# Kernel tuning notes

Hardware: AMD Instinct MI355X
Metric: run time of the kernel (lower is better)

Reference implementation:

```python
import jax, jax.numpy as jnp
import numpy as np
from functools import partial

B, S, V, H, NH, NKV, M, L = 2, 2048, 51200, 1536, 24, 4, 8960, 8
DH = H // NH  # 64
EPS = 1e-6


def setup_inputs() -> dict:
    key = jax.random.key(0)
    ks = jax.random.split(key, 16)
    sc = 0.02
    w = lambda k, shape: jax.random.normal(k, shape, jnp.float32) * sc
    inp = {
        "input_ids": jax.random.randint(ks[0], (B, S), 0, V),
        "attention_mask": jnp.ones((B, S), jnp.float32),
        "embed": w(ks[1], (V, H)),
        "Wq": w(ks[2], (L, H, H)),          "bq": jnp.zeros((L, H), jnp.float32),
        "Wk": w(ks[3], (L, H, NKV * DH)),   "bk": jnp.zeros((L, NKV * DH), jnp.float32),
        "Wv": w(ks[4], (L, H, NKV * DH)),   "bv": jnp.zeros((L, NKV * DH), jnp.float32),
        "Wo": w(ks[5], (L, H, H)),
        "ln1": jnp.ones((L, H), jnp.float32),
        "ln2": jnp.ones((L, H), jnp.float32),
        "Wg": w(ks[6], (L, H, M)),
        "Wu": w(ks[7], (L, H, M)),
        "Wd": w(ks[8], (L, M, H)),
        "norm_w": jnp.ones((H,), jnp.float32),
        "W1": w(ks[9], (H, H)), "b1": jnp.zeros((H,), jnp.float32),
        "W2": w(ks[10], (H, 1)), "b2": jnp.zeros((1,), jnp.float32),
    }
    inv_freq = 1.0 / (10000.0 ** (jnp.arange(0, DH, 2, dtype=jnp.float32) / DH))
    freqs = jnp.outer(jnp.arange(S, dtype=jnp.float32), inv_freq)  # [S, DH/2]
    emb = jnp.concatenate([freqs, freqs], axis=-1)                 # [S, DH]
    inp["cos"] = jnp.cos(emb)
    inp["sin"] = jnp.sin(emb)
    return inp


def _rms(x, w):
    var = jnp.mean(x.astype(jnp.float32) ** 2, axis=-1, keepdims=True)
    return w * (x * jax.lax.rsqrt(var + EPS)).astype(x.dtype)


def _rotate_half(x):
    x1, x2 = jnp.split(x, 2, axis=-1)
    return jnp.concatenate([-x2, x1], axis=-1)


def _forward(input_ids, attention_mask, embed, Wq, bq, Wk, bk, Wv, bv, Wo,
             ln1, ln2, Wg, Wu, Wd, norm_w, W1, b1, W2, b2, cos, sin):
    scale = 1.0 / np.sqrt(DH)
    b, s = input_ids.shape
    c = cos[None, :s, None, :]  # [1,S,1,DH]
    sn = sin[None, :s, None, :]
    rope = lambda t: t * c + _rotate_half(t) * sn
    mask0 = attention_mask[:, None, None, :] == 0  # [B,1,1,S]

    def block(x, p):
        wq, bq_, wk, bk_, wv, bv_, wo, ln1w, ln2w, wg, wu, wd = p
        h = _rms(x, ln1w)
        q = (h @ wq + bq_).reshape(b, s, NH, DH)
        k = (h @ wk + bk_).reshape(b, s, NKV, DH)
        v = (h @ wv + bv_).reshape(b, s, NKV, DH)
        q, k = rope(q), rope(k)
        k = jnp.repeat(k, NH // NKV, axis=2)  # GQA expand to NH heads
        v = jnp.repeat(v, NH // NKV, axis=2)
        scores = jnp.einsum('bqhd,bkhd->bhqk', q, k) * scale
        scores = jnp.where(mask0, -1e10, scores)
        probs = jax.nn.softmax(scores, axis=-1)  # dropout: eval mode (identity)
        attn = jnp.einsum('bhqk,bkhd->bqhd', probs, v).reshape(b, s, H)
        x = x + attn @ wo
        h = _rms(x, ln2w)
        x = x + (jax.nn.sigmoid(h @ wg) * (h @ wu)) @ wd
        return x, None

    x = embed[input_ids]  # [B,S,H]
    x, _ = jax.lax.scan(block, x, (Wq, bq, Wk, bk, Wv, bv, Wo, ln1, ln2, Wg, Wu, Wd))
    x = _rms(x, norm_w)
    h = jax.nn.gelu(x @ W1 + b1, approximate=False)  # torch nn.GELU default = exact
    return h @ W2 + b2  # [B,S,1]


def reference(input_ids, attention_mask, embed, Wq, bq, Wk, bk, Wv, bv, Wo,
              ln1, ln2, Wg, Wu, Wd, norm_w, W1, b1, W2, b2, cos, sin):
    return _forward(input_ids, attention_mask, embed, Wq, bq, Wk, bk, Wv, bv, Wo,
                    ln1, ln2, Wg, Wu, Wd, norm_w, W1, b1, W2, b2, cos, sin)
```

## Files before the change

### kernel.cpp

```cpp
#include <hip/hip_runtime.h>

typedef float f32x4 __attribute__((ext_vector_type(4)));
typedef short s16x8 __attribute__((ext_vector_type(8)));
typedef unsigned short u16;
typedef unsigned short u16x4 __attribute__((ext_vector_type(4)));
typedef unsigned short u16x8 __attribute__((ext_vector_type(8)));
typedef unsigned int u32x2 __attribute__((ext_vector_type(2)));

__device__ __forceinline__ float bf2f(u16 u){ union{unsigned int i; float f;} v; v.i=((unsigned int)u)<<16; return v.f; }
__device__ __forceinline__ u16 f2bf(float f){ union{float f; unsigned int i;} v; v.f=f; return (u16)((v.i + 0x7FFFu + ((v.i>>16)&1u))>>16); }
__device__ __forceinline__ float aexp2(float x){ float r; asm("v_exp_f32 %0, %1" : "=v"(r) : "v"(x)); return r; }
__device__ __forceinline__ unsigned int cvtpk(float lo, float hi){ unsigned int r; asm("v_cvt_pk_bf16_f32 %0, %1, %2" : "=v"(r) : "v"(lo), "v"(hi)); return r; }

#define LOG2E 1.44269504089f

__device__ __forceinline__ void gld16(const void* gp, void* lp){
  __builtin_amdgcn_global_load_lds((__attribute__((address_space(1))) void*)(void*)gp,
                                   (__attribute__((address_space(3))) void*)lp, 16, 0, 0);
}

__device__ __forceinline__ void job_map(int bid, int gridx, int nrt, int nct, int ksplit,
                                        int SR, int SC, int& rt, int& ct, int& ks){
  int jpx = gridx >> 3;
  int wgid = (bid & 7)*jpx + (bid >> 3);
  int nj1 = nrt*nct;
  ks = wgid / nj1; int rr = wgid - ks*nj1;
  int spc = SR*SC, nstc = nct/SC;
  int st = rr / spc, win = rr - st*spc;
  int str_ = st / nstc, stc = st - str_*nstc;
  int wr = win / SC, wc = win - wr*SC;
  rt = str_*SR + wr;
  ct = stc*SC + wc;
}

__global__ __launch_bounds__(256) void k_embed(const int* __restrict__ ids, const float* __restrict__ emb, float* __restrict__ x){
  int r = blockIdx.x;
  int id = ids[r];
  const f32x4* src = (const f32x4*)(emb + (size_t)id*1536);
  f32x4* dst = (f32x4*)(x + (size_t)r*1536);
  for (int i = threadIdx.x; i < 384; i += 256) dst[i] = src[i];
}

__global__ __launch_bounds__(256) void k_mask(const float* __restrict__ mask, u16* __restrict__ mtab){
  int i = blockIdx.x*256 + threadIdx.x;
  float mv = mask[i];
  mtab[i] = (mv==0.f) ? f2bf(-1.4e9f) : f2bf(-4.f*LOG2E);
}

__global__ __launch_bounds__(256) void k_rms(const float* __restrict__ x, const float* __restrict__ w, u16* __restrict__ h){
  int r = blockIdx.x, tid = threadIdx.x;
  const f32x4* xr = (const f32x4*)(x + (size_t)r*1536);
  f32x4 v0 = xr[tid];
  float ss = v0.x*v0.x + v0.y*v0.y + v0.z*v0.z + v0.w*v0.w;
  f32x4 v1 = {0,0,0,0};
  if (tid < 128){ v1 = xr[256+tid]; ss += v1.x*v1.x + v1.y*v1.y + v1.z*v1.z + v1.w*v1.w; }
  #pragma unroll
  for (int off=32; off; off>>=1) ss += __shfl_xor(ss, off, 64);
  __shared__ float red[4];
  if ((tid&63)==0) red[tid>>6] = ss;
  __syncthreads();
  float tot = red[0]+red[1]+red[2]+red[3];
  float invr = rsqrtf(tot*(1.f/1536.f) + 1e-6f);
  const f32x4* w4 = (const f32x4*)w;
  u16x4* h4 = (u16x4*)(h + (size_t)r*1536);
  {
    f32x4 wv = w4[tid];
    u16x4 o; o.x=f2bf(v0.x*invr*wv.x); o.y=f2bf(v0.y*invr*wv.y); o.z=f2bf(v0.z*invr*wv.z); o.w=f2bf(v0.w*invr*wv.w);
    h4[tid] = o;
  }
  if (tid < 128){
    f32x4 wv = w4[256+tid];
    u16x4 o; o.x=f2bf(v1.x*invr*wv.x); o.y=f2bf(v1.y*invr*wv.y); o.z=f2bf(v1.z*invr*wv.z); o.w=f2bf(v1.w*invr*wv.w);
    h4[256+tid] = o;
  }
}

__global__ __launch_bounds__(256) void k_rms_add(float* __restrict__ x, const float* __restrict__ P, const float* __restrict__ w, u16* __restrict__ h){
  int r = blockIdx.x, tid = threadIdx.x;
  f32x4* xr = (f32x4*)(x + (size_t)r*1536);
  const f32x4* pr = (const f32x4*)(P + (size_t)r*1536);
  f32x4 v0 = xr[tid], p0 = pr[tid];
  v0.x+=p0.x; v0.y+=p0.y; v0.z+=p0.z; v0.w+=p0.w;
  xr[tid] = v0;
  float ss = v0.x*v0.x + v0.y*v0.y + v0.z*v0.z + v0.w*v0.w;
  f32x4 v1 = {0,0,0,0};
  if (tid < 128){
    v1 = xr[256+tid]; f32x4 p1 = pr[256+tid];
    v1.x+=p1.x; v1.y+=p1.y; v1.z+=p1.z; v1.w+=p1.w;
    xr[256+tid] = v1;
    ss += v1.x*v1.x + v1.y*v1.y + v1.z*v1.z + v1.w*v1.w;
  }
  #pragma unroll
  for (int off=32; off; off>>=1) ss += __shfl_xor(ss, off, 64);
  __shared__ float red[4];
  if ((tid&63)==0) red[tid>>6] = ss;
  __syncthreads();
  float tot = red[0]+red[1]+red[2]+red[3];
  float invr = rsqrtf(tot*(1.f/1536.f) + 1e-6f);
  const f32x4* w4 = (const f32x4*)w;
  u16x4* h4 = (u16x4*)(h + (size_t)r*1536);
  {
    f32x4 wv = w4[tid];
    u16x4 o; o.x=f2bf(v0.x*invr*wv.x); o.y=f2bf(v0.y*invr*wv.y); o.z=f2bf(v0.z*invr*wv.z); o.w=f2bf(v0.w*invr*wv.w);
    h4[tid] = o;
  }
  if (tid < 128){
    f32x4 wv = w4[256+tid];
    u16x4 o; o.x=f2bf(v1.x*invr*wv.x); o.y=f2bf(v1.y*invr*wv.y); o.z=f2bf(v1.z*invr*wv.z); o.w=f2bf(v1.w*invr*wv.w);
    h4[256+tid] = o;
  }
}

__device__ __forceinline__ void cvt_tile(const float* src, int K, int N, u16* dst, int k0, int n0, int roff, int mode){
  __shared__ float T[64*72];
  int tid = threadIdx.x;
  #pragma unroll
  for (int j=0;j<4;++j){
    int i = tid + j*256;
    int row = i>>4, nf = i&15;
    f32x4 vv = *(const f32x4*)(src + (size_t)(k0+row)*N + n0 + nf*4);
    *(f32x4*)&T[row*72 + nf*4] = vv;
  }
  __syncthreads();
  #pragma unroll
  for (int j=0;j<2;++j){
    int i = tid + j*256;
    int n = i>>3, kc = i&7;
    u16x8 o;
    #pragma unroll
    for (int m=0;m<8;++m) o[m] = f2bf(T[(kc*8+m)*72 + n]);
    int gn = n0 + n;
    int dr = (mode==0) ? (roff + gn) : (((gn>>4)<<5) + ((mode==2)?16:0) + (gn&15));
    *(u16x8*)(dst + (size_t)dr*K + k0 + kc*8) = o;
  }
}

__global__ __launch_bounds__(256) void k_cvt_layer(
  const float* __restrict__ Wq, const float* __restrict__ Wk, const float* __restrict__ Wv,
  const float* __restrict__ Wo, const float* __restrict__ Wg, const float* __restrict__ Wu,
  const float* __restrict__ Wd, u16* qkvt, u16* wot, u16* gut, u16* wdt)
{
  const float* src; int K, N; u16* dst; int roff=0, mode=0;
  switch (blockIdx.y){
    case 0: src=Wq; K=1536; N=1536; dst=qkvt; break;
    case 1: src=Wk; K=1536; N=256;  dst=qkvt; roff=1536; break;
    case 2: src=Wv; K=1536; N=256;  dst=qkvt; roff=1792; break;
    case 3: src=Wo; K=1536; N=1536; dst=wot;  break;
    case 4: src=Wg; K=1536; N=8960; dst=gut;  mode=1; break;
    case 5: src=Wu; K=1536; N=8960; dst=gut;  mode=2; break;
    default: src=Wd; K=8960; N=1536; dst=wdt; break;
  }
  int ntn = N>>6;
  int nt = (K>>6)*ntn;
  int t = blockIdx.x;
  if (t >= nt) return;
  cvt_tile(src, K, N, dst, (t/ntn)<<6, (t%ntn)<<6, roff, mode);
}

__global__ __launch_bounds__(256) void k_cvt_one(const float* __restrict__ src, u16* __restrict__ dst){
  int t = blockIdx.x;
  cvt_tile(src, 1536, 1536, dst, (t/24)<<6, (t%24)<<6, 0, 0);
}

#define MODE_QKV 0
#define MODE_WO 1
#define MODE_GATEUP 2
#define MODE_DOWN 3
#define MODE_W1 4

template<int MODE>
__global__ __launch_bounds__(256) void k_gemm(
  const u16* __restrict__ A, const u16* __restrict__ Bt, int K,
  int nrt, int nct, int ksplit, int klen, int SR, int SC,
  const float* __restrict__ bq_, const float* __restrict__ bk_, const float* __restrict__ bv_,
  float* __restrict__ xio, float* __restrict__ Pf,
  const float* __restrict__ cosT, const float* __restrict__ sinT,
  u16* __restrict__ o0, u16* __restrict__ o1, u16* __restrict__ o2)
{
  int rt, ct, ks;
  job_map(blockIdx.x, gridDim.x, nrt, nct, ksplit, SR, SC, rt, ct, ks);
  int kbase = ks*klen;
  int nt = klen >> 5;

  __shared__ __align__(16) u16 As[3][4096], Bs[3][4096];
  int tid = threadIdx.x;
  int lane = tid & 63, w = tid >> 6;
  int wr = w >> 1, wc = w & 1;
  int row0 = rt * 128, col0 = ct * 128;
  int l15 = lane & 15, l4 = lane >> 4;
  f32x4 acc[4][4] = {};
  const u16* aBase = A + (size_t)row0*K;
  const u16* bBase = Bt + (size_t)col0*K;
  int rr0 = tid & 127, kb0 = tid >> 7;
  int kb1 = kb0 + 2;

  auto stage = [&](int bf, int kt){
    gld16(aBase + (size_t)rr0*K + kt + kb0*8, &As[bf][tid*8]);
    gld16(bBase + (size_t)rr0*K + kt + kb0*8, &Bs[bf][tid*8]);
    gld16(aBase + (size_t)rr0*K + kt + kb1*8, &As[bf][(256+tid)*8]);
    gld16(bBase + (size_t)rr0*K + kt + kb1*8, &Bs[bf][(256+tid)*8]);
  };
  stage(0, kbase); stage(1, kbase+32);

  int bf = 0;
  for (int t = 0; t < nt; ++t){
    if (t < nt-1) asm volatile("s_waitcnt vmcnt(4)" ::: "memory");
    else          asm volatile("s_waitcnt vmcnt(0)" ::: "memory");
    __builtin_amdgcn_s_barrier();
    __builtin_amdgcn_sched_barrier(0);
    if (t+2 < nt){
      int nb = bf+2; if (nb >= 3) nb -= 3;
      stage(nb, kbase + (t+2)*32);
    }
    const u16* Ab = As[bf];
    const u16* Bb = Bs[bf];
    s16x8 af[4], bf_[4];
    #pragma unroll
    for (int i=0;i<4;++i) af[i]  = *(const s16x8*)&Ab[((l4<<7) + wr*64 + i*16 + l15)*8];
    #pragma unroll
    for (int jj=0;jj<4;++jj) bf_[jj] = *(const s16x8*)&Bb[((l4<<7) + wc*64 + jj*16 + l15)*8];
    __builtin_amdgcn_s_setprio(1);
    #pragma unroll
    for (int i=0;i<4;++i)
      #pragma unroll
      for (int jj=0;jj<4;++jj)
        acc[i][jj] = __builtin_amdgcn_mfma_f32_16x16x32_bf16(af[i], bf_[jj], acc[i][jj], 0, 0, 0);
    __builtin_amdgcn_s_setprio(0);
    if (++bf == 3) bf = 0;
  }

  #pragma unroll
  for (int i=0;i<4;++i)
    #pragma unroll
    for (int jj=0;jj<4;++jj)
      #pragma unroll
      for (int r=0;r<4;++r){
        int row = row0 + wr*64 + i*16 + l4*4 + r;
        int c   = col0 + wc*64 + jj*16 + l15;
        float v = acc[i][jj][r];
        if constexpr (MODE == MODE_QKV){
          int b = row >> 11, s = row & 2047;
          if (c < 1536){
            int d = c & 63, hd = c >> 6;
            float vv = v + bq_[c];
            float pv = acc[i][jj^2][r] + bq_[c^32];
            float cv = cosT[s*64+d], sv = sinT[s*64+d];
            float sgn = (d<32) ? -1.f : 1.f;
            float o = (vv*cv + sgn*pv*sv)*(0.125f*LOG2E);
            o0[(size_t)(b*24+hd)*131072 + (size_t)(s>>6)*4096
               + (s&63)*64 + (((d>>3)^(s&7))<<3) + (d&7)] = f2bf(o);
          } else if (c < 1792){
            int c2 = c - 1536, d = c2 & 63, kv = c2 >> 6;
            float vv = v + bk_[c2];
            float pv = acc[i][jj^2][r] + bk_[c2^32];
            float cv = cosT[s*64+d], sv = sinT[s*64+d];
            float sgn = (d<32) ? -1.f : 1.f;
            float o = vv*cv + sgn*pv*sv;
            o1[(size_t)(b*4+kv)*131072 + (size_t)(s>>6)*4096
               + (s&63)*64 + (((d>>3)^(s&7))<<3) + (d&7)] = f2bf(o);
          } else {
            int c2 = c - 1792, d = c2 & 63, kv = c2 >> 6;
            float vv = v + bv_[c2];
            o2[(size_t)(b*4+kv)*131072 + (size_t)(s>>6)*4096
               + d*64 + ((((s>>3)&7)^(d&7))<<3) + (s&7)] = f2bf(vv);
          }
        } else if constexpr (MODE == MODE_WO){
          xio[(size_t)row*1536 + c] += v;
        } else if constexpr (MODE == MODE_W1){
          v += bq_[c];
          float ge = 0.5f * v * (1.f + erff(v * 0.70710678118f));
          o0[(size_t)row*1536 + c] = f2bf(ge);
        }
      }
}

template<int MODE>
__global__ __launch_bounds__(512,2) void k_gemm256(
  const u16* __restrict__ A, const u16* __restrict__ Bt, int K,
  int nrt, int nct, int ksplit, int klen, int SR, int SC,
  float* __restrict__ xio, float* __restrict__ Pf, u16* __restrict__ o0)
{
  int rt, ct, ks;
  job_map(blockIdx.x, gridDim.x, nrt, nct, ksplit, SR, SC, rt, ct, ks);

  __shared__ __align__(16) u16 lds[2][2][16384];
  int tid = threadIdx.x;
  int lane = tid & 63, wid = tid >> 6;
  int wm = wid >> 2, wn = wid & 3;
  int l15 = lane & 15, l4 = lane >> 4;
  int lsw = l15 & 7;
  int row0 = rt*256, col0 = ct*256;
  int kbase = ks*klen*64;

  const u16* aB = A  + (size_t)row0*K + kbase;
  const u16* bB = Bt + (size_t)col0*K + kbase;
  int rsub = tid >> 3;
  int gsw  = (lane & 7) ^ ((lane >> 3) & 7);

  f32x4 acc[8][4] = {};

  auto sgA = [&](int bf, int kt, int c){
    gld16(aB + (size_t)(c*64 + rsub)*K + kt*64 + gsw*8, &lds[bf][0][(c*512+tid)*8]);
  };
  auto sgB = [&](int bf, int kt, int c){
    gld16(bB + (size_t)(c*64 + rsub)*K + kt*64 + gsw*8, &lds[bf][1][(c*512+tid)*8]);
  };

  sgB(0,0,0); sgB(0,0,1); sgB(0,0,2); sgB(0,0,3);
  sgA(0,0,0); sgA(0,0,2); sgA(0,0,1); sgA(0,0,3);

  for (int t = 0; t < klen; ++t){
    int b = t & 1, nb = b ^ 1;
    bool hn = (t+1 < klen);
    const u16* Ab = lds[b][0];
    const u16* Bb = lds[b][1];
    s16x8 bfr[4][2];

    asm volatile("s_waitcnt vmcnt(2)" ::: "memory");
    __builtin_amdgcn_s_barrier();
    __builtin_amdgcn_sched_barrier(0);
    {
      s16x8 af[2][2];
      #pragma unroll
      for (int ii=0;ii<2;++ii)
        #pragma unroll
        for (int ksu=0;ksu<2;++ksu)
          af[ii][ksu] = *(const s16x8*)&Ab[(wm*128 + ii*16 + l15)*64 + (((ksu*4+l4)^lsw)<<3)];
      #pragma unroll
      for (int j=0;j<4;++j)
        #pragma unroll
        for (int ksu=0;ksu<2;++ksu)
          bfr[j][ksu] = *(const s16x8*)&Bb[(wn*64 + j*16 + l15)*64 + (((ksu*4+l4)^lsw)<<3)];
      if (hn){ sgB(nb, t+1, 0); sgB(nb, t+1, 1); }
      asm volatile("s_waitcnt lgkmcnt(0)" ::: "memory");
      __builtin_amdgcn_sched_barrier(0);
      __builtin_amdgcn_s_setprio(1);
      #pragma unroll
      for (int ii=0;ii<2;++ii)
        #pragma unroll
        for (int j=0;j<4;++j)
          #pragma unroll
          for (int ksu=0;ksu<2;++ksu)
            acc[ii][j] = __builtin_amdgcn_mfma_f32_16x16x32_bf16(af[ii][ksu], bfr[j][ksu], acc[ii][j], 0,0,0);
      __builtin_amdgcn_s_setprio(0);
      __builtin_amdgcn_s_barrier();
    }
    {
      s16x8 af[2][2];
      #pragma unroll
      for (int ii=0;ii<2;++ii)
        #pragma unroll
        for (int ksu=0;ksu<2;++ksu)
          af[ii][ksu] = *(const s16x8*)&Ab[(wm*128 + 32 + ii*16 + l15)*64 + (((ksu*4+l4)^lsw)<<3)];
      if (hn){ sgB(nb, t+1, 2); sgB(nb, t+1, 3); }
      asm volatile("s_waitcnt lgkmcnt(0)" ::: "memory");
      __builtin_amdgcn_sched_barrier(0);
      __builtin_amdgcn_s_setprio(1);
      #pragma unroll
      for (int ii=0;ii<2;++ii)
        #pragma unroll
        for (int j=0;j<4;++j)
          #pragma unroll
          for (int ksu=0;ksu<2;++ksu)
            acc[2+ii][j] = __builtin_amdgcn_mfma_f32_16x16x32_bf16(af[ii][ksu], bfr[j][ksu], acc[2+ii][j], 0,0,0);
      __builtin_amdgcn_s_setprio(0);
      __builtin_amdgcn_s_barrier();
    }
    if (hn) asm volatile("s_waitcnt vmcnt(4)" ::: "memory");
    else    asm volatile("s_waitcnt vmcnt(0)" ::: "memory");
    __builtin_amdgcn_s_barrier();
    __builtin_amdgcn_sched_barrier(0);
    {
      s16x8 af[2][2];
      #pragma unroll
      for (int ii=0;ii<2;++ii)
        #pragma unroll
        for (int ksu=0;ksu<2;++ksu)
          af[ii][ksu] = *(const s16x8*)&Ab[(wm*128 + 64 + ii*16 + l15)*64 + (((ksu*4+l4)^lsw)<<3)];
      if (hn){ sgA(nb, t+1, 0); sgA(nb, t+1, 2); }
      asm volatile("s_waitcnt lgkmcnt(0)" ::: "memory");
      __builtin_amdgcn_sched_barrier(0);
      __builtin_amdgcn_s_setprio(1);
      #pragma unroll
      for (int ii=0;ii<2;++ii)
        #pragma unroll
        for (int j=0;j<4;++j)
          #pragma unroll
          for (int ksu=0;ksu<2;++ksu)
            acc[4+ii][j] = __builtin_amdgcn_mfma_f32_16x16x32_bf16(af[ii][ksu], bfr[j][ksu], acc[4+ii][j], 0,0,0);
      __builtin_amdgcn_s_setprio(0);
      __builtin_amdgcn_s_barrier();
    }
    {
      s16x8 af[2][2];
      #pragma unroll
      for (int ii=0;ii<2;++ii)
        #pragma unroll
        for (int ksu=0;ksu<2;++ksu)
          af[ii][ksu] = *(const s16x8*)&Ab[(wm*128 + 96 + ii*16 + l15)*64 + (((ksu*4+l4)^lsw)<<3)];
      if (hn){ sgA(nb, t+1, 1); sgA(nb, t+1, 3); }
      asm volatile("s_waitcnt lgkmcnt(0)" ::: "memory");
      __builtin_amdgcn_sched_barrier(0);
      __builtin_amdgcn_s_setprio(1);
      #pragma unroll
      for (int ii=0;ii<2;++ii)
        #pragma unroll
        for (int j=0;j<4;++j)
          #pragma unroll
          for (int ksu=0;ksu<2;++ksu)
            acc[6+ii][j] = __builtin_amdgcn_mfma_f32_16x16x32_bf16(af[ii][ksu], bfr[j][ksu], acc[6+ii][j], 0,0,0);
      __builtin_amdgcn_s_setprio(0);
      __builtin_amdgcn_s_barrier();
    }
  }

  if constexpr (MODE == MODE_GATEUP){
    #pragma unroll
    for (int i=0;i<8;++i)
      #pragma unroll
      for (int j2=0;j2<4;j2+=2)
        #pragma unroll
        for (int r=0;r<4;++r){
          int row = row0 + wm*128 + i*16 + l4*4 + r;
          int cp  = col0 + wn*64 + j2*16 + l15;
          float gv = acc[i][j2][r], uv = acc[i][j2+1][r];
          float sg = 1.f/(1.f + __expf(-gv));
          int n = ((cp>>5)<<4) + (cp&15);
          o0[(size_t)row*8960 + n] = f2bf(sg*uv);
        }
  } else {
    #pragma unroll
    for (int i=0;i<8;++i)
      #pragma unroll
      for (int j=0;j<4;++j)
        #pragma unroll
        for (int r=0;r<4;++r){
          int row = row0 + wm*128 + i*16 + l4*4 + r;
          int c   = col0 + wn*64 + j*16 + l15;
          float v = acc[i][j][r];
          if (ks == 0) Pf[(size_t)row*1536 + c] = v;
          else         xio[(size_t)row*1536 + c] += v;
        }
  }
}

__global__ __launch_bounds__(256) void k_attn(
  const u16* __restrict__ q, const u16* __restrict__ k, const u16* __restrict__ v,
  const u16* __restrict__ mtab, u16* __restrict__ attn)
{
  __shared__ __align__(16) u16 Qs[4096];
  __shared__ __align__(16) u16 Kd[2][4096];
  __shared__ __align__(16) u16 Vd[2][4096];
  int tid = threadIdx.x;
  int lane = tid & 63, w = tid >> 6;
  int qb = blockIdx.x;
  int bh = blockIdx.y;
  int b = bh / 24, hh = bh % 24, kv = hh / 6;
  int l15 = lane & 15, l4 = lane >> 4;
  int sw = l15 & 7;

  const u16* qhead = q + ((size_t)(b*24 + hh))*131072 + qb*4096;
  const u16* khead = k + ((size_t)(b*4  + kv))*131072;
  const u16* vhead = v + ((size_t)(b*4  + kv))*131072;
  const u16* mrow = mtab + b*2048;

  gld16(qhead + tid*8,       &Qs[tid*8]);
  gld16(qhead + (256+tid)*8, &Qs[(256+tid)*8]);

  auto stage = [&](int bf, int kt){
    gld16(khead + kt*4096 + tid*8,       &Kd[bf][tid*8]);
    gld16(khead + kt*4096 + (256+tid)*8, &Kd[bf][(256+tid)*8]);
    gld16(vhead + kt*4096 + tid*8,       &Vd[bf][tid*8]);
    gld16(vhead + kt*4096 + (256+tid)*8, &Vd[bf][(256+tid)*8]);
  };
  stage(0, 0);

  s16x8 aq0, aq1;
  f32x4 oacc[4] = {};
  float lsum = 0.f;
  u16* Pw = &Qs[w*1024];

  for (int t = 0; t < 32; ++t){
    asm volatile("s_waitcnt vmcnt(0)" ::: "memory");
    __builtin_amdgcn_s_barrier();
    __builtin_amdgcn_sched_barrier(0);
    if (t == 0){
      int qrow = w*16 + l15;
      aq0 = *(const s16x8*)&Qs[qrow*64 + (( l4    ^ sw)<<3)];
      aq1 = *(const s16x8*)&Qs[qrow*64 + (((4+l4) ^ sw)<<3)];
    }
    if (t+1 < 32) stage((t+1)&1, t+1);
    const u16* Kb = Kd[t&1];
    const u16* Vb = Vd[t&1];
    f32x4 sk[4] = {};
    __builtin_amdgcn_s_setprio(1);
    #pragma unroll
    for (int kn=0; kn<4; ++kn){
      int krow = kn*16 + l15;
      s16x8 a0 = *(const s16x8*)&Kb[krow*64 + (( l4    ^ sw)<<3)];
      s16x8 a1 = *(const s16x8*)&Kb[krow*64 + (((4+l4) ^ sw)<<3)];
      sk[kn] = __builtin_amdgcn_mfma_f32_16x16x32_bf16(a0, aq0, sk[kn], 0,0,0);
      sk[kn] = __builtin_amdgcn_mfma_f32_16x16x32_bf16(a1, aq1, sk[kn], 0,0,0);
    }
    __builtin_amdgcn_s_setprio(0);
    #pragma unroll
    for (int kn=0; kn<4; ++kn){
      u16x4 mv = *(const u16x4*)&mrow[t*64 + kn*16 + l4*4];
      float p0 = aexp2(sk[kn][0] + bf2f(mv.x));
      float p1 = aexp2(sk[kn][1] + bf2f(mv.y));
      float p2 = aexp2(sk[kn][2] + bf2f(mv.z));
      float p3 = aexp2(sk[kn][3] + bf2f(mv.w));
      lsum += (p0 + p1) + (p2 + p3);
      u32x2 pk; pk.x = cvtpk(p0, p1); pk.y = cvtpk(p2, p3);
      int g = kn*2 + (l4>>1);
      *(u32x2*)&Pw[l15*64 + ((g ^ sw)<<3) + (l4&1)*4] = pk;
    }
    __builtin_amdgcn_s_setprio(1);
    #pragma unroll
    for (int ksu=0; ksu<2; ++ksu){
      s16x8 ap = *(const s16x8*)&Pw[l15*64 + (((ksu*4+l4) ^ sw)<<3)];
      #pragma unroll
      for (int dg=0; dg<4; ++dg){
        s16x8 bv = *(const s16x8*)&Vb[(dg*16+l15)*64 + (((ksu*4+l4) ^ sw)<<3)];
        oacc[dg] = __builtin_amdgcn_mfma_f32_16x16x32_bf16(ap, bv, oacc[dg], 0,0,0);
      }
    }
    __builtin_amdgcn_s_setprio(0);
  }
  lsum += __shfl_xor(lsum, 16, 64);
  lsum += __shfl_xor(lsum, 32, 64);
  float invq[4];
  #pragma unroll
  for (int r=0;r<4;++r) invq[r] = 1.f / __shfl(lsum, l4*4 + r, 64);
  #pragma unroll
  for (int dg=0;dg<4;++dg)
    #pragma unroll
    for (int r=0;r<4;++r){
      int token = b*2048 + qb*64 + w*16 + l4*4 + r;
      int col = hh*64 + dg*16 + l15;
      attn[(size_t)token*1536 + col] = f2bf(oacc[dg][r] * invq[r]);
    }
}

__global__ __launch_bounds__(256) void k_gemv(const u16* __restrict__ h2, const float* __restrict__ W2, const float* __restrict__ b2, float* __restrict__ out){
  int tid = threadIdx.x, lane = tid & 63, w = tid >> 6;
  int r = blockIdx.x*4 + w;
  const u16* hr = h2 + (size_t)r*1536;
  float s = 0.f;
  #pragma unroll
  for (int i=0;i<24;++i){ int c = lane + i*64; s += bf2f(hr[c]) * W2[c]; }
  #pragma unroll
  for (int off=32; off; off>>=1) s += __shfl_xor(s, off, 64);
  if (lane == 0) out[r] = s + b2[0];
}

extern "C" void kernel_launch(void* const* d_in, const int* in_sizes, int n_in,
                              void* d_out, int out_size, void* d_ws, size_t ws_size,
                              hipStream_t stream)
{
  const int*   ids   = (const int*)d_in[0];
  const float* mask  = (const float*)d_in[1];
  const float* embed = (const float*)d_in[2];
  const float* Wq    = (const float*)d_in[3];
  const float* bq    = (const float*)d_in[4];
  const float* Wk    = (const float*)d_in[5];
  const float* bk    = (const float*)d_in[6];
  const float* Wv    = (const float*)d_in[7];
  const float* bv    = (const float*)d_in[8];
  const float* Wo    = (const float*)d_in[9];
  const float* ln1   = (const float*)d_in[10];
  const float* ln2   = (const float*)d_in[11];
  const float* Wg    = (const float*)d_in[12];
  const float* Wu    = (const float*)d_in[13];
  const float* Wd    = (const float*)d_in[14];
  const float* nw    = (const float*)d_in[15];
  const float* W1    = (const float*)d_in[16];
  const float* b1    = (const float*)d_in[17];
  const float* W2    = (const float*)d_in[18];
  const float* b2    = (const float*)d_in[19];
  const float* cosT  = (const float*)d_in[20];
  const float* sinT  = (const float*)d_in[21];

  char* ws = (char*)d_ws;
  float* x   = (float*)(ws + 0);
  u16* h     = (u16*)(ws + 25165824);
  u16* qb_   = (u16*)(ws + 37748736);
  u16* kb_   = (u16*)(ws + 50331648);
  u16* vb_   = (u16*)(ws + 52428800);
  u16* attn  = (u16*)(ws + 54525952);
  u16* g     = (u16*)(ws + 67108864);
  u16* qkvt  = (u16*)(ws + 140509184);
  u16* wot   = (u16*)(ws + 146800640);
  u16* gut   = (u16*)(ws + 151519232);
  u16* wdt   = (u16*)(ws + 206569472);
  u16* mtab  = (u16*)(ws + 234094592);
  float* Pf  = (float*)(ws + 37748736);
  (void)in_sizes; (void)n_in; (void)out_size; (void)ws_size;

  k_embed<<<4096, 256, 0, stream>>>(ids, embed, x);
  k_mask<<<16, 256, 0, stream>>>(mask, mtab);
  for (int l = 0; l < 8; ++l){
    k_cvt_layer<<<dim3(3360,7), 256, 0, stream>>>(
      Wq + (size_t)l*1536*1536, Wk + (size_t)l*1536*256, Wv + (size_t)l*1536*256,
      Wo + (size_t)l*1536*1536, Wg + (size_t)l*1536*8960, Wu + (size_t)l*1536*8960,
      Wd + (size_t)l*8960*1536, qkvt, wot, gut, wdt);
    if (l == 0) k_rms<<<4096, 256, 0, stream>>>(x, ln1, h);
    else        k_rms_add<<<4096, 256, 0, stream>>>(x, Pf, ln1 + l*1536, h);
    k_gemm<MODE_QKV><<<512, 256, 0, stream>>>(h, qkvt, 1536, 32, 16, 1, 1536, 8, 4,
        bq + l*1536, bk + l*256, bv + l*256, nullptr, nullptr, cosT, sinT, qb_, kb_, vb_);
    k_attn<<<dim3(32,48), 256, 0, stream>>>(qb_, kb_, vb_, mtab, attn);
    k_gemm<MODE_WO><<<384, 256, 0, stream>>>(attn, wot, 1536, 32, 12, 1, 1536, 8, 4,
        nullptr, nullptr, nullptr, x, nullptr, nullptr, nullptr, nullptr, nullptr, nullptr);
    k_rms<<<4096, 256, 0, stream>>>(x, ln2 + l*1536, h);
    k_gemm256<MODE_GATEUP><<<1120, 512, 0, stream>>>(h, gut, 1536, 16, 70, 1, 24, 8, 10,
        nullptr, nullptr, g);
    k_gemm256<MODE_DOWN><<<192, 512, 0, stream>>>(g, wdt, 8960, 16, 6, 2, 70, 4, 6,
        x, Pf, nullptr);
  }
  k_cvt_one<<<576, 256, 0, stream>>>(W1, wot);
  k_rms_add<<<4096, 256, 0, stream>>>(x, Pf, nw, h);
  k_gemm<MODE_W1><<<384, 256, 0, stream>>>(h, wot, 1536, 32, 12, 1, 1536, 8, 4,
      b1, nullptr, nullptr, nullptr, nullptr, nullptr, nullptr, attn, nullptr, nullptr);
  k_gemv<<<1024, 256, 0, stream>>>(attn, W2, b2, (float*)d_out);
}
```

Baseline: 5.326 ms.

## Process 128 query rows per attention block to reuse K/V tiles

Each attention workgroup now handles 128 queries instead of 64, with every wave computing two 16-row query sub-tiles against the same K/V tile loaded from LDS. V fragments are loaded once per k-step and reused across both sub-tiles. This halves the global K/V traffic and the LDS K/V reads per query, and halves the grid to 768 blocks. In exchange it uses more registers and LDS per block, which may lower occupancy and leave less parallelism across the GPU.

```diff
diff --git a/kernel.cpp b/kernel.cpp
--- a/kernel.cpp
+++ b/kernel.cpp
@@ -448,7 +448,7 @@
   const u16* __restrict__ q, const u16* __restrict__ k, const u16* __restrict__ v,
   const u16* __restrict__ mtab, u16* __restrict__ attn)
 {
-  __shared__ __align__(16) u16 Qs[4096];
+  __shared__ __align__(16) u16 Qs[8192];
   __shared__ __align__(16) u16 Kd[2][4096];
   __shared__ __align__(16) u16 Vd[2][4096];
   int tid = threadIdx.x;
@@ -459,13 +459,15 @@
   int l15 = lane & 15, l4 = lane >> 4;
   int sw = l15 & 7;
 
-  const u16* qhead = q + ((size_t)(b*24 + hh))*131072 + qb*4096;
+  const u16* qhead = q + ((size_t)(b*24 + hh))*131072 + qb*8192;
   const u16* khead = k + ((size_t)(b*4  + kv))*131072;
   const u16* vhead = v + ((size_t)(b*4  + kv))*131072;
   const u16* mrow = mtab + b*2048;
 
-  gld16(qhead + tid*8,       &Qs[tid*8]);
-  gld16(qhead + (256+tid)*8, &Qs[(256+tid)*8]);
+  gld16(qhead + tid*8,        &Qs[tid*8]);
+  gld16(qhead + (256+tid)*8,  &Qs[(256+tid)*8]);
+  gld16(qhead + (512+tid)*8,  &Qs[(512+tid)*8]);
+  gld16(qhead + (768+tid)*8,  &Qs[(768+tid)*8]);
 
   auto stage = [&](int bf, int kt){
     gld16(khead + kt*4096 + tid*8,       &Kd[bf][tid*8]);
@@ -475,71 +477,89 @@
   };
   stage(0, 0);
 
-  s16x8 aq0, aq1;
-  f32x4 oacc[4] = {};
-  float lsum = 0.f;
-  u16* Pw = &Qs[w*1024];
+  s16x8 aq[2][2];
+  f32x4 oacc[2][4] = {};
+  float lsum[2] = {0.f, 0.f};
+  u16* Pw = &Qs[w*2048];
 
   for (int t = 0; t < 32; ++t){
     asm volatile("s_waitcnt vmcnt(0)" ::: "memory");
     __builtin_amdgcn_s_barrier();
     __builtin_amdgcn_sched_barrier(0);
     if (t == 0){
-      int qrow = w*16 + l15;
-      aq0 = *(const s16x8*)&Qs[qrow*64 + (( l4    ^ sw)<<3)];
-      aq1 = *(const s16x8*)&Qs[qrow*64 + (((4+l4) ^ sw)<<3)];
+      #pragma unroll
+      for (int qa=0; qa<2; ++qa){
+        int qrow = w*32 + qa*16 + l15;
+        aq[qa][0] = *(const s16x8*)&Qs[qrow*64 + (( l4    ^ sw)<<3)];
+        aq[qa][1] = *(const s16x8*)&Qs[qrow*64 + (((4+l4) ^ sw)<<3)];
+      }
     }
     if (t+1 < 32) stage((t+1)&1, t+1);
     const u16* Kb = Kd[t&1];
     const u16* Vb = Vd[t&1];
-    f32x4 sk[4] = {};
+    f32x4 sk[2][4] = {};
     __builtin_amdgcn_s_setprio(1);
     #pragma unroll
     for (int kn=0; kn<4; ++kn){
       int krow = kn*16 + l15;
       s16x8 a0 = *(const s16x8*)&Kb[krow*64 + (( l4    ^ sw)<<3)];
       s16x8 a1 = *(const s16x8*)&Kb[krow*64 + (((4+l4) ^ sw)<<3)];
-      sk[kn] = __builtin_amdgcn_mfma_f32_16x16x32_bf16(a0, aq0, sk[kn], 0,0,0);
-      sk[kn] = __builtin_amdgcn_mfma_f32_16x16x32_bf16(a1, aq1, sk[kn], 0,0,0);
+      #pragma unroll
+      for (int qa=0; qa<2; ++qa){
+        sk[qa][kn] = __builtin_amdgcn_mfma_f32_16x16x32_bf16(a0, aq[qa][0], sk[qa][kn], 0,0,0);
+        sk[qa][kn] = __builtin_amdgcn_mfma_f32_16x16x32_bf16(a1, aq[qa][1], sk[qa][kn], 0,0,0);
+      }
     }
     __builtin_amdgcn_s_setprio(0);
     #pragma unroll
     for (int kn=0; kn<4; ++kn){
       u16x4 mv = *(const u16x4*)&mrow[t*64 + kn*16 + l4*4];
-      float p0 = aexp2(sk[kn][0] + bf2f(mv.x));
-      float p1 = aexp2(sk[kn][1] + bf2f(mv.y));
-      float p2 = aexp2(sk[kn][2] + bf2f(mv.z));
-      float p3 = aexp2(sk[kn][3] + bf2f(mv.w));
-      lsum += (p0 + p1) + (p2 + p3);
-      u32x2 pk; pk.x = cvtpk(p0, p1); pk.y = cvtpk(p2, p3);
-      int g = kn*2 + (l4>>1);
-      *(u32x2*)&Pw[l15*64 + ((g ^ sw)<<3) + (l4&1)*4] = pk;
+      #pragma unroll
+      for (int qa=0; qa<2; ++qa){
+        float p0 = aexp2(sk[qa][kn][0] + bf2f(mv.x));
+        float p1 = aexp2(sk[qa][kn][1] + bf2f(mv.y));
+        float p2 = aexp2(sk[qa][kn][2] + bf2f(mv.z));
+        float p3 = aexp2(sk[qa][kn][3] + bf2f(mv.w));
+        lsum[qa] += (p0 + p1) + (p2 + p3);
+        u32x2 pk; pk.x = cvtpk(p0, p1); pk.y = cvtpk(p2, p3);
+        int g = kn*2 + (l4>>1);
+        *(u32x2*)&Pw[(qa*16 + l15)*64 + ((g ^ sw)<<3) + (l4&1)*4] = pk;
+      }
     }
     __builtin_amdgcn_s_setprio(1);
     #pragma unroll
     for (int ksu=0; ksu<2; ++ksu){
-      s16x8 ap = *(const s16x8*)&Pw[l15*64 + (((ksu*4+l4) ^ sw)<<3)];
-      #pragma unroll
-      for (int dg=0; dg<4; ++dg){
-        s16x8 bv = *(const s16x8*)&Vb[(dg*16+l15)*64 + (((ksu*4+l4) ^ sw)<<3)];
-        oacc[dg] = __builtin_amdgcn_mfma_f32_16x16x32_bf16(ap, bv, oacc[dg], 0,0,0);
+      s16x8 bv[4];
+      #pragma unroll
+      for (int dg=0; dg<4; ++dg)
+        bv[dg] = *(const s16x8*)&Vb[(dg*16+l15)*64 + (((ksu*4+l4) ^ sw)<<3)];
+      #pragma unroll
+      for (int qa=0; qa<2; ++qa){
+        s16x8 ap = *(const s16x8*)&Pw[(qa*16 + l15)*64 + (((ksu*4+l4) ^ sw)<<3)];
+        #pragma unroll
+        for (int dg=0; dg<4; ++dg)
+          oacc[qa][dg] = __builtin_amdgcn_mfma_f32_16x16x32_bf16(ap, bv[dg], oacc[qa][dg], 0,0,0);
       }
     }
     __builtin_amdgcn_s_setprio(0);
   }
-  lsum += __shfl_xor(lsum, 16, 64);
-  lsum += __shfl_xor(lsum, 32, 64);
-  float invq[4];
-  #pragma unroll
-  for (int r=0;r<4;++r) invq[r] = 1.f / __shfl(lsum, l4*4 + r, 64);
-  #pragma unroll
-  for (int dg=0;dg<4;++dg)
-    #pragma unroll
-    for (int r=0;r<4;++r){
-      int token = b*2048 + qb*64 + w*16 + l4*4 + r;
-      int col = hh*64 + dg*16 + l15;
-      attn[(size_t)token*1536 + col] = f2bf(oacc[dg][r] * invq[r]);
-    }
+  #pragma unroll
+  for (int qa=0; qa<2; ++qa){
+    float t2 = lsum[qa];
+    t2 += __shfl_xor(t2, 16, 64);
+    t2 += __shfl_xor(t2, 32, 64);
+    float invq[4];
+    #pragma unroll
+    for (int r=0;r<4;++r) invq[r] = 1.f / __shfl(t2, l4*4 + r, 64);
+    #pragma unroll
+    for (int dg=0;dg<4;++dg)
+      #pragma unroll
+      for (int r=0;r<4;++r){
+        int token = b*2048 + qb*128 + w*32 + qa*16 + l4*4 + r;
+        int col = hh*64 + dg*16 + l15;
+        attn[(size_t)token*1536 + col] = f2bf(oacc[qa][dg][r] * invq[r]);
+      }
+  }
 }
 
 __global__ __launch_bounds__(256) void k_gemv(const u16* __restrict__ h2, const float* __restrict__ W2, const float* __restrict__ b2, float* __restrict__ out){
@@ -608,7 +628,7 @@
     else        k_rms_add<<<4096, 256, 0, stream>>>(x, Pf, ln1 + l*1536, h);
     k_gemm<MODE_QKV><<<512, 256, 0, stream>>>(h, qkvt, 1536, 32, 16, 1, 1536, 8, 4,
         bq + l*1536, bk + l*256, bv + l*256, nullptr, nullptr, cosT, sinT, qb_, kb_, vb_);
-    k_attn<<<dim3(32,48), 256, 0, stream>>>(qb_, kb_, vb_, mtab, attn);
+    k_attn<<<dim3(16,48), 256, 0, stream>>>(qb_, kb_, vb_, mtab, attn);
     k_gemm<MODE_WO><<<384, 256, 0, stream>>>(attn, wot, 1536, 32, 12, 1, 1536, 8, 4,
         nullptr, nullptr, nullptr, x, nullptr, nullptr, nullptr, nullptr, nullptr, nullptr);
     k_rms<<<4096, 256, 0, stream>>>(x, ln2 + l*1536, h);
```

After: 5.128 ms. 3.7% less time.
